# Kernel optimization log

Measured on AMD Instinct MI355X. Metric: run time of the kernel, lower is better.

## Reference

```python
import jax, jax.numpy as jnp
import numpy as np

B, T, D = 64, 48, 16          # batch, time_depth, input_dim (n variables)
H = 128                       # n_units (== N_units, forced by decomp: y=h_mix has width n_units)
NU = 128                      # N_units
HEADS = 8
HEAD_DIM = H // HEADS
THR = 0.01                    # attention_threshold
LAM = 0.01                    # ridge_lambda
SHORT = 2

# All off-diagonal variable pairs. The torch code gathers only pairs in the batch-union of
# (a_t > 0) & ~eye; using ALL off-diagonal pairs is mathematically identical because excluded
# pairs have a_t == 0 for every batch element, giving all-zero phi columns whose ridge
# coefficients are exactly 0 and which do not perturb the other coefficients or h_hat.
_I, _J = np.nonzero(~np.eye(D, dtype=bool))
I_IDX = jnp.asarray(_I)
J_IDX = jnp.asarray(_J)
P = D * (D - 1)
K = 2 * D + P


def setup_inputs() -> dict:
    key = jax.random.key(0)
    ks = jax.random.split(key, 32)
    f32 = jnp.float32
    n = lambda k, shp, s: (jax.random.normal(k, shp, f32) * s)
    inp = {
        'x': jax.random.normal(ks[0], (B, T, D), f32),
        # per-variable LSTM params
        'W_j': n(ks[1], (D, H, H), 1.0 / np.sqrt(H)),
        'W_i': n(ks[2], (D, H, H), 1.0 / np.sqrt(H)),
        'W_f': n(ks[3], (D, H, H), 1.0 / np.sqrt(H)),
        'W_o': n(ks[4], (D, H, H), 1.0 / np.sqrt(H)),
        'U_j': n(ks[5], (D, 1, H), 0.3),
        'U_i': n(ks[6], (D, 1, H), 0.3),
        'U_f': n(ks[7], (D, 1, H), 0.3),
        'U_o': n(ks[8], (D, 1, H), 0.3),
        'B_j': jnp.full((D, H), 0.01, f32),
        'B_i': jnp.full((D, H), 0.01, f32),
        'B_f': jnp.full((D, H), 0.01, f32),
        'B_o': jnp.full((D, H), 0.01, f32),
        # mix LSTM params
        'u_j': n(ks[9], (D, NU), 0.3),
        'u_i': n(ks[10], (D, NU), 0.3),
        'u_f': n(ks[11], (D, NU), 0.3),
        'u_o': n(ks[12], (D, NU), 0.3),
        'w_j': n(ks[13], (NU, NU), 1.0 / np.sqrt(NU)),
        'w_i': n(ks[14], (NU, NU), 1.0 / np.sqrt(NU)),
        'w_f': n(ks[15], (NU, NU), 1.0 / np.sqrt(NU)),
        'w_o': n(ks[16], (NU, NU), 1.0 / np.sqrt(NU)),
        'b_j': jnp.full((NU,), 0.01, f32),
        'b_i': jnp.full((NU,), 0.01, f32),
        'b_f': jnp.full((NU,), 0.01, f32),
        'b_o': jnp.full((NU,), 0.01, f32),
        # attention params (torch Linear convention: y = x @ W.T)
        'W_qkv': n(ks[17], (3 * H, H), 1.0 / np.sqrt(H)),
        'W_out': n(ks[18], (H, H), 1.0 / np.sqrt(H)),
        # interaction decomposition psi projection
        'W_psi': n(ks[19], (H, H), 1.0 / np.sqrt(H)),
        'b_psi': jnp.full((H,), 0.01, f32),
        # prediction head
        'w_p': n(ks[20], (H, 1), 1.0 / np.sqrt(H)),
        'b_p': jnp.full((1,), 0.01, f32),
    }
    return inp


def _forward(x, W_j, W_i, W_f, W_o, U_j, U_i, U_f, U_o, B_j, B_i, B_f, B_o,
             u_j, u_i, u_f, u_o, w_j, w_i, w_f, w_o, b_j, b_i, b_f, b_o,
             W_qkv, W_out, W_psi, b_psi, w_p, b_p):
    f32 = x.dtype
    eyeK = LAM * jnp.eye(K, dtype=f32)

    def var_gate(h_var, x_t, W, U, Bp):
        # torch einsum('bij,ijk->bik') + einsum('bij,jik->bjk') with x_t unsqueezed
        return jnp.einsum('bdh,dhk->bdk', h_var, W) + x_t[:, :, None] * U[:, 0, :] + Bp

    def step(carry, inp):
        h_var, c_var, h_mix, c_mix = carry
        x_t, t = inp  # x_t: [B, D]
        h_prev = h_var
        # per-variable tensorized LSTM
        j_var = jnp.tanh(var_gate(h_var, x_t, W_j, U_j, B_j))
        i_var = jax.nn.sigmoid(var_gate(h_var, x_t, W_i, U_i, B_i))
        f_var = jax.nn.sigmoid(var_gate(h_var, x_t, W_f, U_f, B_f))
        o_var = jax.nn.sigmoid(var_gate(h_var, x_t, W_o, U_o, B_o))
        c_var = c_var * f_var + i_var * j_var
        h_var = o_var * jnp.tanh(c_var)
        delta_h = h_var - h_prev
        # mix LSTM
        i_t = jax.nn.sigmoid(x_t @ u_i + h_mix @ w_i + b_i)
        f_t = jax.nn.sigmoid(x_t @ u_f + h_mix @ w_f + b_f)
        o_t = jax.nn.sigmoid(x_t @ u_o + h_mix @ w_o + b_o)
        j_t = jnp.tanh(x_t @ u_j + h_mix @ w_j + b_j)
        c_mix = f_t * c_mix + i_t * j_t
        h_mix_lstm = o_t * jnp.tanh(c_mix)
        # multi-head cross-variable attention over the D variables
        qkv = h_var @ W_qkv.T                                  # [B, D, 3H]
        q, k, v = jnp.split(qkv, 3, axis=-1)
        q = q.reshape(B, D, HEADS, HEAD_DIM).transpose(0, 2, 1, 3)
        k = k.reshape(B, D, HEADS, HEAD_DIM).transpose(0, 2, 1, 3)
        v = v.reshape(B, D, HEADS, HEAD_DIM).transpose(0, 2, 1, 3)
        scores = jnp.einsum('bhqe,bhke->bhqk', q, k) / np.sqrt(HEAD_DIM).astype(np.float32)
        attn = jax.nn.softmax(scores, axis=-1)
        attn = jnp.where(attn >= THR, attn, jnp.zeros_like(attn))  # hard threshold, no renorm
        ctx = jnp.einsum('bhqk,bhke->bhqe', attn, v)
        ctx = ctx.transpose(0, 2, 1, 3).reshape(B, D, H)
        z = ctx @ W_out.T                                      # [B, D, H]
        a_t = attn.mean(axis=1)                                # [B, D, D]
        phi_long = jnp.swapaxes(h_prev, 1, 2)                  # [B, H, D]
        phi_short = jnp.swapaxes(delta_h, 1, 2)                # [B, H, D]
        pair = z[:, I_IDX, :] * z[:, J_IDX, :]                 # [B, P, H]
        psi = jnp.tanh(pair @ W_psi.T + b_psi)                 # [B, P, H]
        w = a_t[:, I_IDX, J_IDX][..., None]                    # [B, P, 1]
        phi_inter = jnp.swapaxes(psi * w, 1, 2)                # [B, H, P]
        phi = jnp.concatenate([phi_long, phi_short, phi_inter], axis=2)  # [B, H, K]
        A = jnp.einsum('bhk,bhl->bkl', phi, phi) + eyeK        # [B, K, K]
        bvec = jnp.einsum('bhk,bh->bk', phi, h_mix_lstm)       # [B, K]
        theta = jnp.linalg.solve(A, bvec[..., None])[..., 0]   # [B, K]
        h_hat = jnp.einsum('bhk,bk->bh', phi, theta)           # [B, H]
        alpha = theta[:, :D]
        beta = theta[:, D:2 * D]
        gamma = jnp.zeros((B, D, D), f32).at[:, I_IDX, J_IDX].set(theta[:, 2 * D:])
        pred_y = h_hat @ w_p + b_p                             # [B, 1]
        h_mix_new = jnp.where(t > SHORT, h_hat, h_mix_lstm)
        return (h_var, c_var, h_mix_new, c_mix), (pred_y, alpha, beta, gamma)

    h_var0 = jnp.zeros((B, D, H), f32)
    c_var0 = jnp.zeros((B, D, H), f32)
    h_mix0 = jnp.zeros((B, NU), f32)
    c_mix0 = jnp.zeros((B, NU), f32)
    ts = jnp.arange(T - 1)
    xs = (jnp.swapaxes(x, 0, 1)[:T - 1], ts)
    _, (preds, alphas, betas, gammas) = jax.lax.scan(step, (h_var0, c_var0, h_mix0, c_mix0), xs)
    s = SHORT + 1
    pred = jnp.swapaxes(preds[s:], 0, 1)   # [B, T-SHORT-2, 1]
    return pred, alphas[s:], betas[s:], gammas[s:]


def reference(x, W_j, W_i, W_f, W_o, U_j, U_i, U_f, U_o, B_j, B_i, B_f, B_o,
              u_j, u_i, u_f, u_o, w_j, w_i, w_f, w_o, b_j, b_i, b_f, b_o,
              W_qkv, W_out, W_psi, b_psi, w_p, b_p):
    return _forward(x, W_j, W_i, W_f, W_o, U_j, U_i, U_f, U_o, B_j, B_i, B_f, B_o,
                    u_j, u_i, u_f, u_o, w_j, w_i, w_f, w_o, b_j, b_i, b_f, b_o,
                    W_qkv, W_out, W_psi, b_psi, w_p, b_p)
```

## Files before the change

### kernel.cpp

```cpp
#include <hip/hip_runtime.h>
#include <hip/hip_bf16.h>
#include <math.h>

#define B_ 64
#define T_ 48
#define D_ 16
#define H_ 128
#define NU_ 128
#define LAM_ 0.01f
#define THR_ 0.01f

#define NSTEP_OUT 44
#define OFF_A (B_*NSTEP_OUT)
#define OFF_B (OFF_A + NSTEP_OUT*B_*D_)
#define OFF_G (OFF_B + NSTEP_OUT*B_*D_)

#define PHI_ROWS 240
#define PHI_STR  (PHI_ROWS*H_)
#define PHIBUF   (B_*PHI_STR)
#define GW_STR   12288
#define GBUF     (B_*GW_STR)
#define L_STR    16896
#define LBUF     (B_*L_STR)
#define PLS_STR  4096
// ... 66 lines not shown
            const int half = tid >> 7, mt = tid & 127;
            const float4* w0 = (const float4*)(Wqkv + (size_t)(mt*3 + 0)*H_);
            const float4* w1 = (const float4*)(Wqkv + (size_t)(mt*3 + 1)*H_);
            const float4* w2 = (const float4*)(Wqkv + (size_t)(mt*3 + 2)*H_);
            float acc[3][8] = {};
            for (int i4 = 0; i4 < 32; i4++) {
                float4 wa = w0[i4], wb = w1[i4], wc = w2[i4];
                #pragma unroll
                for (int rr = 0; rr < 8; rr++) {
                    float4 h4 = *(const float4*)&hs[(half*8 + rr)*128 + i4*4];
                    acc[0][rr] += dot4(wa, h4);
                    acc[1][rr] += dot4(wb, h4);
                    acc[2][rr] += dot4(wc, h4);
                }
            }
            #pragma unroll
            for (int q = 0; q < 3; q++)
                #pragma unroll
                for (int rr = 0; rr < 8; rr++)
                    qk[(half*8 + rr)*QKS + mt*3 + q] = acc[q][rr];
        }
        __syncthreads();

        for (int e = tid; e < 2048; e += 256) {
            int hh2 = e >> 8, qd = (e >> 4) & 15, kd = e & 15;
            float s = 0.f;
            #pragma unroll
            for (int e4 = 0; e4 < 4; e4++)
                s += dot4(*(const float4*)&qk[qd*QKS + hh2*16 + e4*4],
                          *(const float4*)&qk[kd*QKS + 128 + hh2*16 + e4*4]);
            sc[hh2*SCS + qd*16 + kd] = s * 0.25f;
        }
        __syncthreads();

        if (tid < 128) {
            int hh2 = tid >> 4, qd = tid & 15;
            float mx = -1e30f;
            #pragma unroll
            for (int kd = 0; kd < 16; kd++) mx = fmaxf(mx, sc[hh2*SCS + qd*16 + kd]);
            float ex[16]; float s = 0.f;
            #pragma unroll
            for (int kd = 0; kd < 16; kd++) { ex[kd] = expf(sc[hh2*SCS + qd*16 + kd] - mx); s += ex[kd]; }
            float inv = 1.0f / s;
            #pragma unroll
            for (int kd = 0; kd < 16; kd++) {
                float a = ex[kd]*inv;
                sc[hh2*SCS + qd*16 + kd] = (a >= THR_) ? a : 0.0f;
            }
        }
        __syncthreads();

        {
            int qd = tid >> 4, kd = tid & 15;
            float s = 0.f;
            #pragma unroll
            for (int hh2 = 0; hh2 < 8; hh2++) s += sc[hh2*SCS + qd*16 + kd];
            at_g[b*256 + qd*16 + kd] = s * 0.125f;
        }

        for (int e = tid; e < 2048; e += 256) {
            int qd = e >> 7, c = e & 127, hh2 = c >> 4, ee = c & 15;
            float s = 0.f;
            #pragma unroll
            for (int kd = 0; kd < 16; kd++) s += sc[hh2*SCS + qd*16 + kd] * qk[kd*QKS + 256 + hh2*16 + ee];
            cx[qd*128 + c] = s;
        }
        __syncthreads();

        {
            int h = tid & 127, half = tid >> 7;
            const float4* wr = (const float4*)(Wout + (size_t)h*H_);
            float acc[8] = {};
            for (int i4 = 0; i4 < 32; i4++) {
                float4 w4 = wr[i4];
                #pragma unroll
                for (int r = 0; r < 8; r++)
                    acc[r] += dot4(w4, *(const float4*)&cx[(half*8 + r)*128 + i4*4]);
            }
            #pragma unroll
            for (int r = 0; r < 8; r++) z[b*2048 + (half*8 + r)*H_ + h] = acc[r];
        }
    } else if (bx < 256) {
        const int tg = t + 1;
        if (tg < 3 || tg > T_ - 2) return;
        const int tile = (bx - 64) >> 6, b = (bx - 64) & 63;
        const int r0 = (tile >= 1) ? 64 : 0;
        const int c0 = (tile == 2) ? 64 : 0;
        const bool diag = (r0 == c0);
        float* prt = smem;
        float* pct = smem + 1024;
        const float* pb   = phi + ((size_t)(tg%3))*PHIBUF + (size_t)b*PHI_STR;
        const float* plsb = pls + ((size_t)(tg&3))*PLSBUF + (size_t)b*PLS_STR;
        const int tr = tid >> 4, tc = tid & 15;
        const int kk = tid >> 4, rr4 = (tid & 15) << 2;
        float acc[4][4] = {};
        float4 vr, vc;

        {
            const float* src = (kk < 32) ? (plsb + (size_t)kk*H_) : (pb + (size_t)(kk - 32)*H_);
            vr = *(const float4*)&src[r0 + rr4];
            if (!diag) vc = *(const float4*)&src[c0 + rr4];
        }
        for (int kt = 0; kt < 17; kt++) {
            *(float4*)&prt[kk*64 + rr4] = vr;
            if (!diag) *(float4*)&pct[kk*64 + rr4] = vc;
            __syncthreads();
            if (kt < 16) {
                int krow = (kt + 1)*16 + kk;
                const float* src = (krow < 32) ? (plsb + (size_t)krow*H_)
                                               : (pb + (size_t)(krow - 32)*H_);
                vr = *(const float4*)&src[r0 + rr4];
                if (!diag) vc = *(const float4*)&src[c0 + rr4];
            }
            const float* pcb = diag ? prt : pct;
            #pragma unroll
            for (int k2 = 0; k2 < 16; k2++) {
                float4 a4 = *(const float4*)&prt[k2*64 + tr*4];
                float4 b4 = *(const float4*)&pcb[k2*64 + tc*4];
                float av[4] = {a4.x, a4.y, a4.z, a4.w};
                float bv[4] = {b4.x, b4.y, b4.z, b4.w};
                #pragma unroll
                for (int i = 0; i < 4; i++)
                    #pragma unroll
                    for (int j = 0; j < 4; j++)
                        acc[i][j] += av[i]*bv[j];
            }
            __syncthreads();
        }
        float* Gt = Gring + ((size_t)(tg&1))*GBUF + (size_t)b*GW_STR + (size_t)tile*4096;
        #pragma unroll
        for (int i = 0; i < 4; i++) {
            int lr = tr*4 + i;
            float v[4];
            #pragma unroll
            for (int j = 0; j < 4; j++) {
                int lc = tc*4 + j;
                v[j] = acc[i][j] + ((diag && lr == lc) ? LAM_ : 0.0f);
            }
            float4 o; o.x = v[0]; o.y = v[1]; o.z = v[2]; o.w = v[3];
            *(float4*)&Gt[lr*64 + tc*4] = o;
        }
    } else {
        const int tv = t - 1;
        if (tv < 0 || tv > T_ - 2) return;
        const int b = bx - 256;
        if (tv < 3) {
            if (tid < 128) h_mix[b*128 + tid] = hml[b*128 + tid];
            return;
        }
        float* ys = smem;
        const float* Lb = Lring + ((size_t)(tv&1))*LBUF + (size_t)b*L_STR;

        if (tid < 64) {
            __builtin_amdgcn_s_setprio(1);
            const int lane = tid;
            float hm0 = hml[b*128 + lane];
            float hm1 = hml[b*128 + lane + 64];
            float dv0 = Lb[lane*132 + 128];
            float dv1 = Lb[(lane+64)*132 + 128];
            float acc0 = hm0, acc1 = hm1;

            {
                float c0[16], c1[16], n0[16], n1[16];
                #pragma unroll
                for (int k = 0; k < 16; ++k) {
                    c0[k] = Lb[k*132 + lane];
                    c1[k] = Lb[k*132 + lane + 64];
                }
                for (int g = 0; g < 4; ++g) {
                    if (g < 3) {
                        #pragma unroll
                        for (int k = 0; k < 16; ++k) {
                            n0[k] = Lb[(16*(g+1)+k)*132 + lane];
                            n1[k] = Lb[(16*(g+1)+k)*132 + lane + 64];
                        }
                    }
                    const int s = 16*g;
                    #pragma unroll
                    for (int k = 0; k < 16; ++k) {
                        int j = s + k;
                        float yj = rdlane(acc0 * dv0, j);
                        if (lane > j) acc0 -= c0[k]*yj;
                        else if (lane == j) acc0 = yj;
                        acc1 -= c1[k]*yj;
                    }
                    #pragma unroll
                    for (int k = 0; k < 16; ++k) { c0[k] = n0[k]; c1[k] = n1[k]; }
                }
            }
            {
                float c1[16], n1[16];
                #pragma unroll
                for (int k = 0; k < 16; ++k) c1[k] = Lb[(64+k)*132 + lane + 64];
                for (int g = 0; g < 4; ++g) {
                    if (g < 3) {
                        #pragma unroll
                        for (int k = 0; k < 16; ++k)
                            n1[k] = Lb[(64+16*(g+1)+k)*132 + lane + 64];
                    }
                    #pragma unroll
                    for (int k = 0; k < 16; ++k) {
                        int j = 16*g + k;
                        float yj = rdlane(acc1 * dv1, j);
                        if (lane > j) acc1 -= c1[k]*yj;
                        else if (lane == j) acc1 = yj;
                    }
                    #pragma unroll
                    for (int k = 0; k < 16; ++k) c1[k] = n1[k];
                }
            }
            ys[lane] = acc0;
            ys[lane + 64] = acc1;

            for (int p = 7; p >= 0; --p) {
                const int s = p*16;
                float br = 0.f, minv = 0.f;
                float lc[16];
                if (lane < 16) {
                    br = ys[s + lane];
                    minv = Lb[(s+lane)*132 + 128];
                    #pragma unroll
                    for (int k4 = 0; k4 < 4; ++k4) {
                        float4 f4 = *(const float4*)&Lb[(s+lane)*132 + s + k4*4];
                        lc[k4*4+0]=f4.x; lc[k4*4+1]=f4.y; lc[k4*4+2]=f4.z; lc[k4*4+3]=f4.w;
                    }
                } else {
                    #pragma unroll
                    for (int k = 0; k < 16; ++k) lc[k] = 0.f;
                }
                float xk[16];
                #pragma unroll
                for (int j = 15; j >= 0; --j) {
                    if (lane == j) br *= minv;
                    float xj = rdlane(br, j);
                    if (lane < j) br -= lc[j]*xj;
                    xk[j] = xj;
                }
                if (lane < 16) ys[s + lane] = br;
                for (int i = lane; i < s; i += 64) {
                    float a = ys[i];
                    #pragma unroll
                    for (int k4 = 0; k4 < 4; ++k4) {
                        float4 f4 = *(const float4*)&Lb[i*132 + s + k4*4];
                        a -= f4.x*xk[k4*4] + f4.y*xk[k4*4+1] + f4.z*xk[k4*4+2] + f4.w*xk[k4*4+3];
                    }
                    ys[i] = a;
                }
            }

            float y0 = ys[lane], y1 = ys[lane + 64];
            float hh0 = hm0 - LAM_*y0, hh1 = hm1 - LAM_*y1;
            h_mix[b*128 + lane]      = hh0;
            h_mix[b*128 + lane + 64] = hh1;
            float pw = hh0 * w_p[lane] + hh1 * w_p[lane + 64];
            for (int off = 32; off; off >>= 1) pw += __shfl_down(pw, off);
            if (lane == 0) out[b*NSTEP_OUT + (tv - 3)] = pw + b_p[0];
            __builtin_amdgcn_s_setprio(0);
        }
        __syncthreads();

        {
            const int ts = tv - 3;
            const float* plsb = pls + ((size_t)(tv&3))*PLSBUF + (size_t)b*PLS_STR;
            const float* phb  = phi + ((size_t)(tv%3))*PHIBUF + (size_t)b*PHI_STR;
            const float4* y4  = (const float4*)ys;
            for (int k = tid; k < 272; k += 256) {
                const float* rowp = (k < 32) ? plsb + (size_t)k*H_
                                             : phb + (size_t)(k - 32)*H_;
                const float4* r4 = (const float4*)rowp;
                float th = 0.f;
                #pragma unroll
                for (int i4 = 0; i4 < 32; i4++) th += dot4(r4[i4], y4[i4]);
                if (k < 16)
                    out[OFF_A + ts*(B_*D_) + b*D_ + k] = th;
                else if (k < 32)
                    out[OFF_B + ts*(B_*D_) + b*D_ + (k - 16)] = th;
                else {
                    int p = k - 32, ip = p/15, jj = p%15, jp = jj + (jj >= ip ? 1 : 0);
                    out[OFF_G + ts*(B_*D_*D_) + b*(D_*D_) + ip*D_ + jp] = th;
                }
            }
            if (tid < D_)
                out[OFF_G + ts*(B_*D_*D_) + b*(D_*D_) + tid*D_ + tid] = 0.0f;
        }
    }
}

__global__ __launch_bounds__(256) void k_Q(
    const float* __restrict__ z, const float* __restrict__ at,
    const float* __restrict__ Wpsi, const float* __restrict__ bpsi,
    float* __restrict__ phi,
    const float* __restrict__ x, const float* __restrict__ hv,
    const float* __restrict__ Wj, const float* __restrict__ Wi, const float* __restrict__ Wf, const float* __restrict__ Wo,
    const float* __restrict__ Uj, const float* __restrict__ Ui, const float* __restrict__ Uf, const float* __restrict__ Uo,
    const float* __restrict__ Bj, const float* __restrict__ Bi, const float* __restrict__ Bf, const float* __restrict__ Bo,
    float* __restrict__ gates,
    const float* __restrict__ Gring, float* __restrict__ Lring,
    const float* __restrict__ h_mix, float* __restrict__ c_mix, float* __restrict__ hml,
    const float* __restrict__ uj, const float* __restrict__ ui, const float* __restrict__ uf, const float* __restrict__ uo,
    const float* __restrict__ wj, const float* __restrict__ wi, const float* __restrict__ wf, const float* __restrict__ wo,
    const float* __restrict__ bj, const float* __restrict__ bi, const float* __restrict__ bf_, const float* __restrict__ bo,
    int t)
{
    __shared__ __align__(16) float smem[16896];
    const int tid = threadIdx.x;
    const int bx = blockIdx.x;

    if (bx < 128) {
        const int tf = t + (bx >> 6);
        if ((t & 1) || tf < 3 || tf > T_ - 2) return;
        const int b = bx & 63;
        float* Ac = smem;

        const int R = tid >> 4, C = tid & 15;
        const bool lower = (C <= R);

        float g[8][8] = {};
        if (lower) {
            const int tsel = (C >= 8) ? 2 : ((R >= 8) ? 1 : 0);
            const float* Gt = Gring + ((size_t)(tf&1))*GBUF + (size_t)b*GW_STR + (size_t)tsel*4096;
            const int lcb = C*8 - ((C >= 8) ? 64 : 0);
            #pragma unroll
            for (int r = 0; r < 8; ++r) {
                const int lr = R*8 + r - ((R >= 8) ? 64 : 0);
                float4 lo = *(const float4*)(Gt + lr*64 + lcb);
                float4 hi = *(const float4*)(Gt + lr*64 + lcb + 4);
                g[r][0]=lo.x; g[r][1]=lo.y; g[r][2]=lo.z; g[r][3]=lo.w;
                g[r][4]=hi.x; g[r][5]=hi.y; g[r][6]=hi.z; g[r][7]=hi.w;
            }
        }

        for (int p = 0; p < 8; ++p) {
            const int s = p*16;
            if ((C >> 1) == p && R >= 2*p) {
                #pragma unroll
                for (int c = 0; c < 8; ++c) {
                    float4 lo = {g[0][c], g[1][c], g[2][c], g[3][c]};
                    float4 hi = {g[4][c], g[5][c], g[6][c], g[7][c]};
                    *(float4*)&Ac[(C*8 + c)*132 + R*8]     = lo;
                    *(float4*)&Ac[(C*8 + c)*132 + R*8 + 4] = hi;
                }
            }
            __syncthreads();
            if (tid < 64) {
                const int lane = tid;
                const int r0 = s + lane, r1 = r0 + 64;
                const bool v0 = r0 < 128, v1 = r1 < 128;
                float a0[16], a1[16];
                #pragma unroll
                for (int k = 0; k < 16; ++k) {
                    a0[k] = v0 ? Ac[(s+k)*132 + r0] : 0.f;
                    a1[k] = v1 ? Ac[(s+k)*132 + r1] : 0.f;
                }
                float myinv = 0.f;
                #pragma unroll
                for (int j = 0; j < 16; ++j) {
                    float piv = rdlane(a0[j], j);
                    float inv = rsqrtf(piv);
                    float dsq = piv * inv;
                    if (lane == j) myinv = inv;
                    a0[j] = (lane == j) ? dsq : a0[j]*inv;
                    a1[j] *= inv;
                    #pragma unroll
                    for (int c = j+1; c < 16; ++c) {
                        float Lcj = rdlane(a0[j], c);
                        a0[c] -= a0[j]*Lcj;
                        a1[c] -= a1[j]*Lcj;
                    }
                }
                if (lane < 16) Ac[(s+lane)*132 + 128] = myinv;
                #pragma unroll
                for (int k = 0; k < 16; ++k) {
                    if (v0) Ac[(s+k)*132 + r0] = a0[k];
                    if (v1) Ac[(s+k)*132 + r1] = a1[k];
                }
            }
            __syncthreads();
            if (lower && C >= 2*(p+1)) {
                const float* colp = &Ac[s*132];
                float4 r04 = *(const float4*)&colp[R*8];
                float4 r14 = *(const float4*)&colp[R*8 + 4];
                float4 c04 = *(const float4*)&colp[C*8];
                float4 c14 = *(const float4*)&colp[C*8 + 4];
                #pragma unroll
                for (int k = 0; k < 16; ++k) {
                    float lr[8] = {r04.x,r04.y,r04.z,r04.w,r14.x,r14.y,r14.z,r14.w};
                    float lc[8] = {c04.x,c04.y,c04.z,c04.w,c14.x,c14.y,c14.z,c14.w};
                    if (k < 15) {
                        const float* coln = &Ac[(s+k+1)*132];
                        r04 = *(const float4*)&coln[R*8];
                        r14 = *(const float4*)&coln[R*8 + 4];
                        c04 = *(const float4*)&coln[C*8];
                        c14 = *(const float4*)&coln[C*8 + 4];
                    }
                    #pragma unroll
                    for (int r = 0; r < 8; ++r)
                        #pragma unroll
                        for (int c = 0; c < 8; ++c)
                            g[r][c] -= lr[r]*lc[c];
                }
            }
        }
        __syncthreads();
        {
            float* Lb = Lring + ((size_t)(tf&1))*LBUF + (size_t)b*L_STR;
            const float4* s4 = (const float4*)Ac;
            float4* d4 = (float4*)Lb;
            for (int e = tid; e < 4224; e += 256) d4[e] = s4[e];
        }
    } else if (bx < 448) {
        const int tp = t + 2;
        if (tp < 3 || tp > T_ - 2) return;
        const int pc = (bx - 128) >> 6, b = (bx - 128) & 63;
        const int p0 = pc * 48;
        float* zs = smem;
        float* pr = smem + 2048;

        {
            const float4* zsrc = (const float4*)(z + b*2048);
            #pragma unroll
            for (int i = 0; i < 2; ++i) ((float4*)zs)[i*256 + tid] = zsrc[i*256 + tid];
        }
        __syncthreads();
        for (int e = tid; e < 48*128; e += 256) {
            int pp = e >> 7, c = e & 127;
            int p = p0 + pp, ip = p/15, jj2 = p%15, jp = jj2 + (jj2 >= ip ? 1 : 0);
            pr[pp*128 + c] = zs[ip*128 + c] * zs[jp*128 + c];
        }
        __syncthreads();

        const int hg = tid & 31, pg = tid >> 5;
        const int h0 = hg*4, pp0 = pg*6;
        const float4* w0 = (const float4*)(Wpsi + (size_t)(h0+0)*H_);
        const float4* w1 = (const float4*)(Wpsi + (size_t)(h0+1)*H_);
        const float4* w2 = (const float4*)(Wpsi + (size_t)(h0+2)*H_);
        const float4* w3 = (const float4*)(Wpsi + (size_t)(h0+3)*H_);
        float acc[6][4] = {};
        for (int i4 = 0; i4 < 32; i4++) {
            float4 wa = w0[i4], wb = w1[i4], wc = w2[i4], wd = w3[i4];
            #pragma unroll
            for (int r = 0; r < 6; r++) {
                float4 p4 = *(const float4*)&pr[(pp0 + r)*128 + i4*4];
                acc[r][0] += dot4(wa, p4);
                acc[r][1] += dot4(wb, p4);
                acc[r][2] += dot4(wc, p4);
                acc[r][3] += dot4(wd, p4);
            }
        }
        float4 bb = *(const float4*)&bpsi[h0];
        float* phb = phi + ((size_t)(tp%3))*PHIBUF + (size_t)b*PHI_STR;
        #pragma unroll
        for (int r = 0; r < 6; r++) {
            int pp = pp0 + r, p = p0 + pp;
            int ip = p/15, jj2 = p%15, jp = jj2 + (jj2 >= ip ? 1 : 0);
            float wat = at[b*256 + ip*16 + jp];
            float4 o;
            o.x = tanhf(acc[r][0] + bb.x) * wat;
            o.y = tanhf(acc[r][1] + bb.y) * wat;
            o.z = tanhf(acc[r][2] + bb.z) * wat;
            o.w = tanhf(acc[r][3] + bb.w) * wat;
            *(float4*)&phb[(size_t)p*H_ + h0] = o;
        }
    } else if (bx < 576) {
        const int tn = t + 3;
        if (tn < 0 || tn > T_ - 2) return;
        float* hsT = smem;
        float* Ws  = smem + 8704;
        const int fbx = bx - 448;
        const int kh = fbx & 1, g = (fbx >> 1) & 3, d = fbx >> 3;
        const int k0 = kh * 64;
        const float* W  = (g==0?Wj:(g==1?Wi:(g==2?Wf:Wo))) + (size_t)d*H_*H_;
        const float* U  = (g==0?Uj:(g==1?Ui:(g==2?Uf:Uo))) + d*H_;
        const float* Bp = (g==0?Bj:(g==1?Bi:(g==2?Bf:Bo))) + d*H_;

        for (int e = tid; e < 64*128; e += 256) {
            int b2 = e >> 7, h2 = e & 127;
            hsT[h2*68 + b2] = hv[(b2*D_ + d)*H_ + h2];
        }
        const int tb = tid >> 4, tk = tid & 15;
        float acc[4][4] = {};

        for (int hc = 0; hc < 2; hc++) {
            __syncthreads();
            for (int e = tid; e < 64*64; e += 256) {
                int h2 = e >> 6, kk = e & 63;
                Ws[h2*64 + kk] = W[(hc*64 + h2)*H_ + k0 + kk];
            }
            __syncthreads();
            for (int h2 = 0; h2 < 64; h2++) {
                float4 hb = *(const float4*)&hsT[(hc*64 + h2)*68 + tb*4];
                float4 wk = *(const float4*)&Ws[h2*64 + tk*4];
                float hbv[4] = {hb.x, hb.y, hb.z, hb.w};
                float wkv[4] = {wk.x, wk.y, wk.z, wk.w};
                #pragma unroll
                for (int a2 = 0; a2 < 4; a2++)
                    #pragma unroll
                    for (int c2 = 0; c2 < 4; c2++)
                        acc[a2][c2] += hbv[a2] * wkv[c2];
            }
        }

        float u4[4], bp4[4];
        #pragma unroll
        for (int c2 = 0; c2 < 4; c2++) { u4[c2] = U[k0 + tk*4 + c2]; bp4[c2] = Bp[k0 + tk*4 + c2]; }

        #pragma unroll
        for (int a2 = 0; a2 < 4; a2++) {
            int b2 = tb*4 + a2;
            float xv = x[(b2*T_ + tn)*D_ + d];
            float4 o;
            float pre[4];
            #pragma unroll
            for (int c2 = 0; c2 < 4; c2++) pre[c2] = acc[a2][c2] + xv*u4[c2] + bp4[c2];
            if (g == 0) { o.x = tanhf(pre[0]); o.y = tanhf(pre[1]); o.z = tanhf(pre[2]); o.w = tanhf(pre[3]); }
            else        { o.x = sigm(pre[0]);  o.y = sigm(pre[1]);  o.z = sigm(pre[2]);  o.w = sigm(pre[3]); }
            *(float4*)&gates[(size_t)g*(B_*D_*H_) + (b2*D_ + d)*H_ + k0 + tk*4] = o;
        }
    } else {
        const int tm = t;
        if (tm < 0 || tm > T_ - 2) return;
        const int b = bx - 576;
        float* xs  = smem;
        float* hs2 = smem + 16;
        float* gj  = smem + 144;
        float* gi  = smem + 272;
        float* gf  = smem + 400;
        float* go  = smem + 528;
        const int n = tid & 127, gg = tid >> 7;
        if (tid < 16)  xs[tid]  = x[(b*T_ + tm)*D_ + tid];
        if (tid < 128) hs2[tid] = h_mix[b*NU_ + tid];
        __syncthreads();

        const float* uA = gg ? uf : uj;
        const float* uB = gg ? uo : ui;
        const float* wA = gg ? wf : wj;
        const float* wB = gg ? wo : wi;
        float accA = gg ? bf_[n] : bj[n];
        float accB = gg ? bo[n]  : bi[n];
        #pragma unroll
        for (int d2 = 0; d2 < 16; ++d2) {
            float xv = xs[d2];
            accA += xv * uA[d2*NU_ + n];
            accB += xv * uB[d2*NU_ + n];
        }
        for (int m = 0; m < 128; ++m) {
            float hvv = hs2[m];
            accA += hvv * wA[m*NU_ + n];
            accB += hvv * wB[m*NU_ + n];
        }
        if (gg == 0) { gj[n] = tanhf(accA); gi[n] = sigm(accB); }
        else         { gf[n] = sigm(accA);  go[n] = sigm(accB); }
        __syncthreads();
        if (tid < 128) {
            float cn = gf[tid]*c_mix[b*NU_ + tid] + gi[tid]*gj[tid];
            c_mix[b*NU_ + tid] = cn;
            hml[b*NU_ + tid]   = go[tid]*tanhf(cn);
        }
    }
}


__global__ __launch_bounds__(256) void k_X8(
    float* __restrict__ hv, float* __restrict__ cv,
    const float* __restrict__ gates, float* __restrict__ pls,
    const float* __restrict__ Wqkv, const float* __restrict__ Wout,
    float* __restrict__ z, float* __restrict__ at_g,
    const float* __restrict__ phi, float* __restrict__ Gw,
    const float* __restrict__ x, const float* __restrict__ h_mix,
    float* __restrict__ c_mix, float* __restrict__ hml,
    const float* __restrict__ uj, const float* __restrict__ ui, const float* __restrict__ uf, const float* __restrict__ uo,
    const float* __restrict__ wj, const float* __restrict__ wi, const float* __restrict__ wf, const float* __restrict__ wo,
    const float* __restrict__ bj, const float* __restrict__ bi, const float* __restrict__ bf_, const float* __restrict__ bo,
    const float* __restrict__ ybuf, float* __restrict__ out,
    int ta, int tg, int tm, int te)
{
    __shared__ __align__(16) float smem[12416];
    const int tid = threadIdx.x;
    const int bx = blockIdx.x;

    if (bx < 64) {
        if (ta < 0) return;
        const int b = bx;
        const int BDH = B_*D_*H_;
        float* hs = smem;
        float* qk = smem + 2048;
        float* sc = smem + 8256;
        float* cx = smem + 10368;

        float* plsb = pls + ((size_t)(ta&3)*B_ + b)*PLS_STR;
        const float4* g0 = (const float4*)(gates + b*2048);
        const float4* g1 = (const float4*)(gates + BDH + b*2048);
        const float4* g2 = (const float4*)(gates + 2*BDH + b*2048);
        const float4* g3 = (const float4*)(gates + 3*BDH + b*2048);
        float4* cv4 = (float4*)(cv + b*2048);
        float4* hv4 = (float4*)(hv + b*2048);
        float4* pl0 = (float4*)plsb;
        float4* pl1 = (float4*)(plsb + 16*H_);
        #pragma unroll
        for (int i = 0; i < 2; ++i) {
            int e4 = i*256 + tid;
            float4 jv = g0[e4], iv = g1[e4], fv = g2[e4], ov = g3[e4];
            float4 c = cv4[e4], ho = hv4[e4];
            float4 cn, hn, dl;
            cn.x = c.x*fv.x + iv.x*jv.x; hn.x = ov.x*tanhf(cn.x); dl.x = hn.x - ho.x;
            cn.y = c.y*fv.y + iv.y*jv.y; hn.y = ov.y*tanhf(cn.y); dl.y = hn.y - ho.y;
            cn.z = c.z*fv.z + iv.z*jv.z; hn.z = ov.z*tanhf(cn.z); dl.z = hn.z - ho.z;
            cn.w = c.w*fv.w + iv.w*jv.w; hn.w = ov.w*tanhf(cn.w); dl.w = hn.w - ho.w;
            cv4[e4] = cn; hv4[e4] = hn;
            ((float4*)hs)[e4] = hn;
            pl0[e4] = ho;
            pl1[e4] = dl;
        }
        __syncthreads();
        {
            const int half = tid >> 7, mt = tid & 127;
            const float4* w0 = (const float4*)(Wqkv + (size_t)(mt*3 + 0)*H_);
            const float4* w1 = (const float4*)(Wqkv + (size_t)(mt*3 + 1)*H_);
            const float4* w2 = (const float4*)(Wqkv + (size_t)(mt*3 + 2)*H_);
            float acc[3][8] = {};
            for (int i4 = 0; i4 < 32; i4++) {
                float4 wa = w0[i4], wb = w1[i4], wc = w2[i4];
                #pragma unroll
                for (int rr = 0; rr < 8; rr++) {
                    float4 h4 = *(const float4*)&hs[(half*8 + rr)*128 + i4*4];
                    acc[0][rr] += dot4(wa, h4);
                    acc[1][rr] += dot4(wb, h4);
                    acc[2][rr] += dot4(wc, h4);
                }
            }
            #pragma unroll
            for (int q = 0; q < 3; q++)
                #pragma unroll
                for (int rr = 0; rr < 8; rr++)
                    qk[(half*8 + rr)*QKS + mt*3 + q] = acc[q][rr];
        }
        __syncthreads();
        for (int e = tid; e < 2048; e += 256) {
            int hh2 = e >> 8, qd = (e >> 4) & 15, kd = e & 15;
            float s = 0.f;
            #pragma unroll
            for (int e4 = 0; e4 < 4; e4++)
                s += dot4(*(const float4*)&qk[qd*QKS + hh2*16 + e4*4],
                          *(const float4*)&qk[kd*QKS + 128 + hh2*16 + e4*4]);
            sc[hh2*SCS + qd*16 + kd] = s * 0.25f;
        }
        __syncthreads();
        if (tid < 128) {
            int hh2 = tid >> 4, qd = tid & 15;
            float mx = -1e30f;
            #pragma unroll
            for (int kd = 0; kd < 16; kd++) mx = fmaxf(mx, sc[hh2*SCS + qd*16 + kd]);
            float ex[16]; float s = 0.f;
            #pragma unroll
            for (int kd = 0; kd < 16; kd++) { ex[kd] = expf(sc[hh2*SCS + qd*16 + kd] - mx); s += ex[kd]; }
            float inv = 1.0f / s;
            #pragma unroll
            for (int kd = 0; kd < 16; kd++) {
                float a = ex[kd]*inv;
                sc[hh2*SCS + qd*16 + kd] = (a >= THR_) ? a : 0.0f;
            }
        }
        __syncthreads();
        {
            int qd = tid >> 4, kd = tid & 15;
            float s = 0.f;
            #pragma unroll
            for (int hh2 = 0; hh2 < 8; hh2++) s += sc[hh2*SCS + qd*16 + kd];
            at_g[b*256 + qd*16 + kd] = s * 0.125f;
        }
        for (int e = tid; e < 2048; e += 256) {
            int qd = e >> 7, c = e & 127, hh2 = c >> 4, ee = c & 15;
            float s = 0.f;
            #pragma unroll
            for (int kd = 0; kd < 16; kd++) s += sc[hh2*SCS + qd*16 + kd] * qk[kd*QKS + 256 + hh2*16 + ee];
            cx[qd*128 + c] = s;
        }
        __syncthreads();
        {
            int h = tid & 127, half = tid >> 7;
            const float4* wr = (const float4*)(Wout + (size_t)h*H_);
            float acc[8] = {};
            for (int i4 = 0; i4 < 32; i4++) {
                float4 w4 = wr[i4];
                #pragma unroll
                for (int r = 0; r < 8; r++)
                    acc[r] += dot4(w4, *(const float4*)&cx[(half*8 + r)*128 + i4*4]);
            }
            #pragma unroll
            for (int r = 0; r < 8; r++) z[b*2048 + (half*8 + r)*H_ + h] = acc[r];
        }
    } else if (bx < 256) {
        if (tg < 0) return;
        const int tile = (bx - 64) >> 6, b = (bx - 64) & 63;
        const int r0 = (tile >= 1) ? 64 : 0;
        const int c0 = (tile == 2) ? 64 : 0;
        const bool diag = (r0 == c0);
        float* prt = smem;
        float* pct = smem + 1024;
        const float* pb   = phi + (size_t)(tg&1)*PHIBUF + (size_t)b*PHI_STR;
        const float* plsb = pls + ((size_t)(tg&3)*B_ + b)*PLS_STR;
        const int tr = tid >> 4, tc = tid & 15;
        float acc[4][4] = {};
        for (int kt = 0; kt < 17; kt++) {
            __syncthreads();
            for (int e = tid; e < 16*64; e += 256) {
                int kk = e >> 6, rr = e & 63;
                int krow = kt*16 + kk;
                const float* src = (krow < 32) ? (plsb + (size_t)krow*H_)
                                               : (pb + (size_t)(krow - 32)*H_);
                prt[kk*64 + rr] = src[r0 + rr];
                if (!diag) pct[kk*64 + rr] = src[c0 + rr];
            }
            __syncthreads();
            const float* pcb = diag ? prt : pct;
            #pragma unroll
            for (int kk = 0; kk < 16; kk++) {
                float4 a4 = *(const float4*)&prt[kk*64 + tr*4];
                float4 b4 = *(const float4*)&pcb[kk*64 + tc*4];
                float av[4] = {a4.x, a4.y, a4.z, a4.w};
                float bv[4] = {b4.x, b4.y, b4.z, b4.w};
                #pragma unroll
                for (int i = 0; i < 4; i++)
                    #pragma unroll
                    for (int j = 0; j < 4; j++)
                        acc[i][j] += av[i]*bv[j];
            }
        }
        float* Gt = Gw + (size_t)b*GW_STR + (size_t)tile*4096;
        #pragma unroll
        for (int i = 0; i < 4; i++) {
            int lr = tr*4 + i;
            float v[4];
            #pragma unroll
            for (int j = 0; j < 4; j++) {
                int lc = tc*4 + j;
                v[j] = acc[i][j] + ((diag && lr == lc) ? LAM_ : 0.0f);
            }
            float4 o; o.x = v[0]; o.y = v[1]; o.z = v[2]; o.w = v[3];
            *(float4*)&Gt[lr*64 + tc*4] = o;
        }
    } else if (bx < 320) {
        if (tm < 0) return;
        const int b = bx - 256;
        float* xs  = smem;
        float* hs2 = smem + 16;
        float* gj  = smem + 144;
        float* gi  = smem + 272;
        float* gf  = smem + 400;
        float* go  = smem + 528;
        const int n = tid & 127, gg = tid >> 7;
        if (tid < 16)  xs[tid]  = x[(b*T_ + tm)*D_ + tid];
        if (tid < 128) hs2[tid] = h_mix[b*NU_ + tid];
        __syncthreads();
        const float* uA = gg ? uf : uj;
        const float* uB = gg ? uo : ui;
        const float* wA = gg ? wf : wj;
        const float* wB = gg ? wo : wi;
        float accA = gg ? bf_[n] : bj[n];
        float accB = gg ? bo[n]  : bi[n];
        #pragma unroll
        for (int d2 = 0; d2 < 16; ++d2) {
            float xv = xs[d2];
            accA += xv * uA[d2*NU_ + n];
            accB += xv * uB[d2*NU_ + n];
        }
        for (int m = 0; m < 128; ++m) {
            float hvv = hs2[m];
            accA += hvv * wA[m*NU_ + n];
            accB += hvv * wB[m*NU_ + n];
        }
        if (gg == 0) { gj[n] = tanhf(accA); gi[n] = sigm(accB); }
        else         { gf[n] = sigm(accA);  go[n] = sigm(accB); }
        __syncthreads();
        if (tid < 128) {
            float cn = gf[tid]*c_mix[b*NU_ + tid] + gi[tid]*gj[tid];
            c_mix[b*NU_ + tid] = cn;
            hml[b*NU_ + tid]   = go[tid]*tanhf(cn);
        }
    } else {
        if (te < 3) return;
        const int eb = bx - 320, b = eb >> 1, half = eb & 1;
        const int ts = te - 3;
        float* ys = smem;
        if (tid < 128) ys[tid] = ybuf[b*128 + tid];
        __syncthreads();
        const int k = half*136 + tid;
        if (tid < 136) {
            const float* rowp = (k < 32)
                ? pls + ((size_t)(te&3)*B_ + b)*PLS_STR + (size_t)k*H_
                : phi + (size_t)(te&1)*PHIBUF + (size_t)b*PHI_STR + (size_t)(k - 32)*H_;
            const float4* r4 = (const float4*)rowp;
            const float4* y4 = (const float4*)ys;
            float th = 0.f;
// ... 434 lines not shown
```

Baseline: 3.171 ms.

## Halve k_Q shared memory by panel-only Cholesky staging and chunked LSTM loads

The Cholesky branch now keeps only the current 16-column panel in shared memory and writes each factored panel straight to the global L ring, instead of staging the whole 128x132 factor and copying it out at the end. The LSTM gate branch loads the transposed hidden state in two 64-row chunks alongside the weight chunks rather than all at once. Together these halve the kernel's static shared memory, which could allow more resident blocks per CU. In exchange, global stores are now scattered per panel from 64 threads, and the hidden-state load is split into two phases.

```diff
diff --git a/kernel.cpp b/kernel.cpp
--- a/kernel.cpp
+++ b/kernel.cpp
@@ -392,7 +392,7 @@
     const float* __restrict__ bj, const float* __restrict__ bi, const float* __restrict__ bf_, const float* __restrict__ bo,
     int t)
 {
-    __shared__ __align__(16) float smem[16896];
+    __shared__ __align__(16) float smem[8448];
     const int tid = threadIdx.x;
     const int bx = blockIdx.x;
 
@@ -400,7 +400,7 @@
         const int tf = t + (bx >> 6);
         if ((t & 1) || tf < 3 || tf > T_ - 2) return;
         const int b = bx & 63;
-        float* Ac = smem;
+        float* Pan = smem;
 
         const int R = tid >> 4, C = tid & 15;
         const bool lower = (C <= R);
@@ -420,15 +420,18 @@
             }
         }
 
+        float* Lb = Lring + ((size_t)(tf&1))*LBUF + (size_t)b*L_STR;
+
         for (int p = 0; p < 8; ++p) {
             const int s = p*16;
             if ((C >> 1) == p && R >= 2*p) {
                 #pragma unroll
                 for (int c = 0; c < 8; ++c) {
+                    const int lc = ((C & 1) << 3) + c;
                     float4 lo = {g[0][c], g[1][c], g[2][c], g[3][c]};
                     float4 hi = {g[4][c], g[5][c], g[6][c], g[7][c]};
-                    *(float4*)&Ac[(C*8 + c)*132 + R*8]     = lo;
-                    *(float4*)&Ac[(C*8 + c)*132 + R*8 + 4] = hi;
+                    *(float4*)&Pan[lc*132 + R*8]     = lo;
+                    *(float4*)&Pan[lc*132 + R*8 + 4] = hi;
                 }
             }
             __syncthreads();
@@ -439,8 +442,8 @@
                 float a0[16], a1[16];
                 #pragma unroll
                 for (int k = 0; k < 16; ++k) {
-                    a0[k] = v0 ? Ac[(s+k)*132 + r0] : 0.f;
-                    a1[k] = v1 ? Ac[(s+k)*132 + r1] : 0.f;
+                    a0[k] = v0 ? Pan[k*132 + r0] : 0.f;
+                    a1[k] = v1 ? Pan[k*132 + r1] : 0.f;
                 }
                 float myinv = 0.f;
                 #pragma unroll
@@ -458,16 +461,16 @@
                         a1[c] -= a1[j]*Lcj;
                     }
                 }
-                if (lane < 16) Ac[(s+lane)*132 + 128] = myinv;
+                if (lane < 16) Lb[(s+lane)*132 + 128] = myinv;
                 #pragma unroll
                 for (int k = 0; k < 16; ++k) {
-                    if (v0) Ac[(s+k)*132 + r0] = a0[k];
-                    if (v1) Ac[(s+k)*132 + r1] = a1[k];
+                    if (v0) { Pan[k*132 + r0] = a0[k]; Lb[(s+k)*132 + r0] = a0[k]; }
+                    if (v1) { Pan[k*132 + r1] = a1[k]; Lb[(s+k)*132 + r1] = a1[k]; }
                 }
             }
             __syncthreads();
             if (lower && C >= 2*(p+1)) {
-                const float* colp = &Ac[s*132];
+                const float* colp = Pan;
                 float4 r04 = *(const float4*)&colp[R*8];
                 float4 r14 = *(const float4*)&colp[R*8 + 4];
                 float4 c04 = *(const float4*)&colp[C*8];
@@ -477,7 +480,7 @@
                     float lr[8] = {r04.x,r04.y,r04.z,r04.w,r14.x,r14.y,r14.z,r14.w};
                     float lc[8] = {c04.x,c04.y,c04.z,c04.w,c14.x,c14.y,c14.z,c14.w};
                     if (k < 15) {
-                        const float* coln = &Ac[(s+k+1)*132];
+                        const float* coln = &Pan[(k+1)*132];
                         r04 = *(const float4*)&coln[R*8];
                         r14 = *(const float4*)&coln[R*8 + 4];
                         c04 = *(const float4*)&coln[C*8];
@@ -490,13 +493,7 @@
                             g[r][c] -= lr[r]*lc[c];
                 }
             }
-        }
-        __syncthreads();
-        {
-            float* Lb = Lring + ((size_t)(tf&1))*LBUF + (size_t)b*L_STR;
-            const float4* s4 = (const float4*)Ac;
-            float4* d4 = (float4*)Lb;
-            for (int e = tid; e < 4224; e += 256) d4[e] = s4[e];
+            __syncthreads();
         }
     } else if (bx < 448) {
         const int tp = t + 2;
@@ -555,7 +552,7 @@
         const int tn = t + 3;
         if (tn < 0 || tn > T_ - 2) return;
         float* hsT = smem;
-        float* Ws  = smem + 8704;
+        float* Ws  = smem + 4352;
         const int fbx = bx - 448;
         const int kh = fbx & 1, g = (fbx >> 1) & 3, d = fbx >> 3;
         const int k0 = kh * 64;
@@ -563,22 +560,22 @@
         const float* U  = (g==0?Uj:(g==1?Ui:(g==2?Uf:Uo))) + d*H_;
         const float* Bp = (g==0?Bj:(g==1?Bi:(g==2?Bf:Bo))) + d*H_;
 
-        for (int e = tid; e < 64*128; e += 256) {
-            int b2 = e >> 7, h2 = e & 127;
-            hsT[h2*68 + b2] = hv[(b2*D_ + d)*H_ + h2];
-        }
         const int tb = tid >> 4, tk = tid & 15;
         float acc[4][4] = {};
 
         for (int hc = 0; hc < 2; hc++) {
             __syncthreads();
             for (int e = tid; e < 64*64; e += 256) {
+                int b2 = e >> 6, h2 = e & 63;
+                hsT[h2*68 + b2] = hv[(b2*D_ + d)*H_ + hc*64 + h2];
+            }
+            for (int e = tid; e < 64*64; e += 256) {
                 int h2 = e >> 6, kk = e & 63;
                 Ws[h2*64 + kk] = W[(hc*64 + h2)*H_ + k0 + kk];
             }
             __syncthreads();
             for (int h2 = 0; h2 < 64; h2++) {
-                float4 hb = *(const float4*)&hsT[(hc*64 + h2)*68 + tb*4];
+                float4 hb = *(const float4*)&hsT[h2*68 + tb*4];
                 float4 wk = *(const float4*)&Ws[h2*64 + tk*4];
                 float hbv[4] = {hb.x, hb.y, hb.z, hb.w};
                 float wkv[4] = {wk.x, wk.y, wk.z, wk.w};
```

Measured after the change: 3.367 ms. 6.2% more time.
